# Kernel optimization log

Hardware: AMD Instinct MI355X
Metric: run time of the kernel (lower is better)

## Reference

```python
import jax, jax.numpy as jnp
import numpy as np

E = 16           # num_experts
K = 2            # top-k
NOISE_STD = 1.0 / E
TAU = 1.0
EPS = 1e-8


def setup_inputs() -> dict:
    key = jax.random.key(0)
    k1, k2, k3, k4 = jax.random.split(key, 4)
    B, C, H, W = 128, 512, 32, 32
    x = jax.random.normal(k1, (B, C, H, W), dtype=jnp.float32)
    # nn.Linear(dim, num_experts, bias=False): weight [E, C]
    W_gate = jax.random.normal(k2, (E, C), dtype=jnp.float32) * (1.0 / np.sqrt(C))
    comp = jax.random.uniform(k3, (E,), dtype=jnp.float32, minval=0.5, maxval=1.5)
    complexity = comp / comp.max()  # complexity_scale == 'max'
    noise = jax.random.normal(k4, (B, E), dtype=jnp.float32) * NOISE_STD
    return {"x": x, "W_gate": W_gate, "complexity": complexity, "noise": noise}


def _std_unbiased(a):
    # torch .std() uses ddof=1
    return jnp.std(a, ddof=1)


def _norm_cdf(z):
    return 0.5 * (1.0 + jax.lax.erf(z / np.sqrt(2.0).astype(np.float32)))


def reference(x, W_gate, complexity, noise):
    B = x.shape[0]
    # gate: AdaptiveAvgPool2d(1) -> [B,C] -> Linear -> [B,E]
    pooled = x.mean(axis=(2, 3))                     # [B, C]
    logits = pooled @ W_gate.T                       # [B, E]

    # importance loss (training path)
    importance = jax.nn.softmax(logits, axis=-1).sum(axis=0) * (complexity * TAU)  # [E]
    loss_imp = (_std_unbiased(importance) / (importance.mean() + EPS)) ** 2

    noisy_logits = logits + noise                    # [B, E]
    gating_scores = jax.nn.softmax(noisy_logits, axis=-1)
    top_k_values, top_k_indices = jax.lax.top_k(gating_scores, K)   # [B, K]

    # load loss: prob each expert's noisy logit beats the k-th noisy logit
    _, noisy_idx = jax.lax.top_k(noisy_logits, K)
    thr = jnp.take_along_axis(noisy_logits, noisy_idx[:, K - 1:K], axis=-1)  # [B,1]
    noise_required = (thr - logits) / NOISE_STD      # [B, E]
    p = 1.0 - _norm_cdf(noise_required)
    p_mean = p.mean(axis=0)                          # [E]
    loss_load = (_std_unbiased(p_mean) / (p_mean.mean() + EPS)) ** 2

    aux_loss = 0.5 * loss_imp + 0.5 * loss_load

    # scatter top-k values back into dense [B, E] gates
    rows = jnp.arange(B)[:, None]
    gates = jnp.zeros_like(logits).at[rows, top_k_indices].set(top_k_values)
    return gates, top_k_indices, top_k_values, aux_loss
```

## Files before the change

### kernel.cpp

```cpp
#include <hip/hip_runtime.h>
#include <math.h>

#define BB 128
#define CC 512
#define HW 1024
#define EE 16
#define KK 2
#define INV_NOISE_STD 16.0f
#define EPSV 1e-8f

typedef float vf4 __attribute__((ext_vector_type(4)));

__device__ __forceinline__ float wave_sum(float v) {
    #pragma unroll
    for (int off = 32; off > 0; off >>= 1) v += __shfl_down(v, off, 64);
    return v;
}

__global__ void __launch_bounds__(256) pool_kernel(const float* __restrict__ x,
                                                   float* __restrict__ pooled) {
    int wave = (blockIdx.x * 256 + threadIdx.x) >> 6;
    int lane = threadIdx.x & 63;
    const vf4* p = (const vf4*)(x + (size_t)wave * HW);
    float s = 0.0f;
    #pragma unroll
    for (int j = 0; j < 4; ++j) {
        vf4 v = __builtin_nontemporal_load(&p[lane + 64 * j]);
        s += (v.x + v.y) + (v.z + v.w);
    }
    s = wave_sum(s);
    if (lane == 0) pooled[wave] = s * (1.0f / 1024.0f);
}

__global__ void __launch_bounds__(256) logits_kernel(const float* __restrict__ pooled,
                                                     const float* __restrict__ Wg,
                                                     float* __restrict__ logits) {
    __shared__ float prow[CC];
    int b = blockIdx.x;
    for (int c = threadIdx.x; c < CC; c += 256) prow[c] = pooled[b * CC + c];
    __syncthreads();
    int t = threadIdx.x;
    int e = t >> 4;
    int g = t & 15;
    float s = 0.0f;
    for (int c = g; c < CC; c += 16) s += prow[c] * Wg[e * CC + c];
    #pragma unroll
    for (int off = 8; off > 0; off >>= 1) s += __shfl_down(s, off, 16);
    if (g == 0) logits[b * EE + e] = s;
}

__global__ void __launch_bounds__(128) stats_kernel(const float* __restrict__ logits,
                                                    const float* __restrict__ complexity,
                                                    const float* __restrict__ noise,
                                                    float* __restrict__ out) {
    __shared__ float imp[EE];
    __shared__ float psum[EE];
    int t = threadIdx.x;
    int lane = t & 63;
    if (t < EE) { imp[t] = 0.0f; psum[t] = 0.0f; }
    __syncthreads();

    int b = t;
    float lg[EE], nlg[EE];
    #pragma unroll
    for (int e = 0; e < EE; ++e) lg[e] = logits[b * EE + e];
    #pragma unroll
    for (int e = 0; e < EE; ++e) nlg[e] = lg[e] + noise[b * EE + e];

    float mx = lg[0];
    #pragma unroll
    for (int e = 1; e < EE; ++e) mx = fmaxf(mx, lg[e]);
    float sm[EE]; float se = 0.0f;
    #pragma unroll
    for (int e = 0; e < EE; ++e) { sm[e] = expf(lg[e] - mx); se += sm[e]; }
    float inv_se = 1.0f / se;
    #pragma unroll
    for (int e = 0; e < EE; ++e) {
        float ws = wave_sum(sm[e] * inv_se);
        if (lane == 0) atomicAdd(&imp[e], ws);
    }

    float mxn = nlg[0];
    #pragma unroll
    for (int e = 1; e < EE; ++e) mxn = fmaxf(mxn, nlg[e]);
    float gsc[EE]; float sen = 0.0f;
    #pragma unroll
    for (int e = 0; e < EE; ++e) { gsc[e] = expf(nlg[e] - mxn); sen += gsc[e]; }
    float inv_sen = 1.0f / sen;
    #pragma unroll
    for (int e = 0; e < EE; ++e) gsc[e] *= inv_sen;

    int i1 = 0;
    #pragma unroll
    for (int e = 1; e < EE; ++e) if (nlg[e] > nlg[i1]) i1 = e;
    int i2 = (i1 == 0) ? 1 : 0;
    #pragma unroll
    for (int e = 0; e < EE; ++e) if (e != i1 && e != i2 && nlg[e] > nlg[i2]) i2 = e;
    float thr = nlg[i2];
    float v1 = gsc[i1], v2 = gsc[i2];

    #pragma unroll
    for (int e = 0; e < EE; ++e) {
        float z = (thr - lg[e]) * INV_NOISE_STD;
        float p = 0.5f * erfcf(z * 0.70710678118654752f);
        float ws = wave_sum(p);
        if (lane == 0) atomicAdd(&psum[e], ws);
    }

    #pragma unroll
    for (int e = 0; e < EE; ++e)
        out[b * EE + e] = (e == i1) ? v1 : ((e == i2) ? v2 : 0.0f);
    out[BB * EE + b * KK + 0] = (float)i1;
    out[BB * EE + b * KK + 1] = (float)i2;
    out[BB * EE + BB * KK + b * KK + 0] = v1;
    out[BB * EE + BB * KK + b * KK + 1] = v2;

    __syncthreads();
    if (t == 0) {
        float im[EE]; float mean1 = 0.0f;
        #pragma unroll
        for (int e = 0; e < EE; ++e) { im[e] = imp[e] * complexity[e]; mean1 += im[e]; }
        mean1 *= (1.0f / EE);
        float var1 = 0.0f;
        #pragma unroll
        for (int e = 0; e < EE; ++e) { float d = im[e] - mean1; var1 += d * d; }
        var1 *= (1.0f / (EE - 1));
        float li = var1 / ((mean1 + EPSV) * (mean1 + EPSV));

        float pm[EE]; float mean2 = 0.0f;
        #pragma unroll
        for (int e = 0; e < EE; ++e) { pm[e] = psum[e] * (1.0f / BB); mean2 += pm[e]; }
        mean2 *= (1.0f / EE);
        float var2 = 0.0f;
        #pragma unroll
        for (int e = 0; e < EE; ++e) { float d = pm[e] - mean2; var2 += d * d; }
        var2 *= (1.0f / (EE - 1));
        float ll = var2 / ((mean2 + EPSV) * (mean2 + EPSV));

        out[BB * EE + 2 * BB * KK] = 0.5f * li + 0.5f * ll;
    }
}

extern "C" void kernel_launch(void* const* d_in, const int* in_sizes, int n_in,
                              void* d_out, int out_size, void* d_ws, size_t ws_size,
                              hipStream_t stream) {
    const float* x     = (const float*)d_in[0];
    const float* Wg    = (const float*)d_in[1];
    const float* comp  = (const float*)d_in[2];
    const float* noise = (const float*)d_in[3];
    float* out = (float*)d_out;

    float* pooled = (float*)d_ws;
    float* logits = pooled + BB * CC;

    pool_kernel<<<(BB * CC) / 4, 256, 0, stream>>>(x, pooled);
    logits_kernel<<<BB, 256, 0, stream>>>(pooled, Wg, logits);
    stats_kernel<<<1, 128, 0, stream>>>(logits, comp, noise, out);
}
```

Measured before the change: 356.4 us.

## Fuse logits GEMV and stats into a single one-block kernel

Merges the logits kernel and the stats kernel into one 1024-thread single-block kernel. It loops over the batch in groups of 4 rows, keeps the logits in shared memory and then runs the softmax, top-k and loss stats. This removes one kernel launch and the global round-trip of the logits. In exchange the 128-block GEMV now runs serially in one block over 32 iterations with barriers, so that phase gets longer. The total is dominated by the 256MB pooling pass.

```diff
diff --git a/kernel.cpp b/kernel.cpp
--- a/kernel.cpp
+++ b/kernel.cpp
@@ -32,108 +32,112 @@
     if (lane == 0) pooled[wave] = s * (1.0f / 1024.0f);
 }
 
-__global__ void __launch_bounds__(256) logits_kernel(const float* __restrict__ pooled,
+__global__ void __launch_bounds__(1024) fused_kernel(const float* __restrict__ pooled,
                                                      const float* __restrict__ Wg,
-                                                     float* __restrict__ logits) {
-    __shared__ float prow[CC];
-    int b = blockIdx.x;
-    for (int c = threadIdx.x; c < CC; c += 256) prow[c] = pooled[b * CC + c];
-    __syncthreads();
-    int t = threadIdx.x;
-    int e = t >> 4;
-    int g = t & 15;
-    float s = 0.0f;
-    for (int c = g; c < CC; c += 16) s += prow[c] * Wg[e * CC + c];
-    #pragma unroll
-    for (int off = 8; off > 0; off >>= 1) s += __shfl_down(s, off, 16);
-    if (g == 0) logits[b * EE + e] = s;
-}
-
-__global__ void __launch_bounds__(128) stats_kernel(const float* __restrict__ logits,
-                                                    const float* __restrict__ complexity,
-                                                    const float* __restrict__ noise,
-                                                    float* __restrict__ out) {
+                                                     const float* __restrict__ complexity,
+                                                     const float* __restrict__ noise,
+                                                     float* __restrict__ out) {
+    __shared__ float lsm[BB * EE];
+    __shared__ float prow[4 * CC];
     __shared__ float imp[EE];
     __shared__ float psum[EE];
     int t = threadIdx.x;
-    int lane = t & 63;
+
     if (t < EE) { imp[t] = 0.0f; psum[t] = 0.0f; }
-    __syncthreads();
 
-    int b = t;
-    float lg[EE], nlg[EE];
-    #pragma unroll
-    for (int e = 0; e < EE; ++e) lg[e] = logits[b * EE + e];
-    #pragma unroll
-    for (int e = 0; e < EE; ++e) nlg[e] = lg[e] + noise[b * EE + e];
-
-    float mx = lg[0];
-    #pragma unroll
-    for (int e = 1; e < EE; ++e) mx = fmaxf(mx, lg[e]);
-    float sm[EE]; float se = 0.0f;
-    #pragma unroll
-    for (int e = 0; e < EE; ++e) { sm[e] = expf(lg[e] - mx); se += sm[e]; }
-    float inv_se = 1.0f / se;
-    #pragma unroll
-    for (int e = 0; e < EE; ++e) {
-        float ws = wave_sum(sm[e] * inv_se);
-        if (lane == 0) atomicAdd(&imp[e], ws);
+    int sub = t >> 8;
+    int tt  = t & 255;
+    int e   = tt >> 4;
+    int g   = tt & 15;
+    for (int b0 = 0; b0 < BB; b0 += 4) {
+        for (int c = t; c < 4 * CC; c += 1024)
+            prow[c] = pooled[(size_t)b0 * CC + c];
+        __syncthreads();
+        float s = 0.0f;
+        for (int c = g; c < CC; c += 16) s += prow[sub * CC + c] * Wg[e * CC + c];
+        #pragma unroll
+        for (int off = 8; off > 0; off >>= 1) s += __shfl_down(s, off, 16);
+        if (g == 0) lsm[(b0 + sub) * EE + e] = s;
+        __syncthreads();
     }
 
-    float mxn = nlg[0];
-    #pragma unroll
-    for (int e = 1; e < EE; ++e) mxn = fmaxf(mxn, nlg[e]);
-    float gsc[EE]; float sen = 0.0f;
-    #pragma unroll
-    for (int e = 0; e < EE; ++e) { gsc[e] = expf(nlg[e] - mxn); sen += gsc[e]; }
-    float inv_sen = 1.0f / sen;
-    #pragma unroll
-    for (int e = 0; e < EE; ++e) gsc[e] *= inv_sen;
+    if (t < BB) {
+        int b = t;
+        int lane = t & 63;
+        float lg[EE], nlg[EE];
+        #pragma unroll
+        for (int e2 = 0; e2 < EE; ++e2) lg[e2] = lsm[b * EE + e2];
+        #pragma unroll
+        for (int e2 = 0; e2 < EE; ++e2) nlg[e2] = lg[e2] + noise[b * EE + e2];
 
-    int i1 = 0;
-    #pragma unroll
-    for (int e = 1; e < EE; ++e) if (nlg[e] > nlg[i1]) i1 = e;
-    int i2 = (i1 == 0) ? 1 : 0;
-    #pragma unroll
-    for (int e = 0; e < EE; ++e) if (e != i1 && e != i2 && nlg[e] > nlg[i2]) i2 = e;
-    float thr = nlg[i2];
-    float v1 = gsc[i1], v2 = gsc[i2];
+        float mx = lg[0];
+        #pragma unroll
+        for (int e2 = 1; e2 < EE; ++e2) mx = fmaxf(mx, lg[e2]);
+        float sm[EE]; float se = 0.0f;
+        #pragma unroll
+        for (int e2 = 0; e2 < EE; ++e2) { sm[e2] = expf(lg[e2] - mx); se += sm[e2]; }
+        float inv_se = 1.0f / se;
+        #pragma unroll
+        for (int e2 = 0; e2 < EE; ++e2) {
+            float ws = wave_sum(sm[e2] * inv_se);
+            if (lane == 0) atomicAdd(&imp[e2], ws);
+        }
 
-    #pragma unroll
-    for (int e = 0; e < EE; ++e) {
-        float z = (thr - lg[e]) * INV_NOISE_STD;
-        float p = 0.5f * erfcf(z * 0.70710678118654752f);
-        float ws = wave_sum(p);
-        if (lane == 0) atomicAdd(&psum[e], ws);
+        float mxn = nlg[0];
+        #pragma unroll
+        for (int e2 = 1; e2 < EE; ++e2) mxn = fmaxf(mxn, nlg[e2]);
+        float gsc[EE]; float sen = 0.0f;
+        #pragma unroll
+        for (int e2 = 0; e2 < EE; ++e2) { gsc[e2] = expf(nlg[e2] - mxn); sen += gsc[e2]; }
+        float inv_sen = 1.0f / sen;
+        #pragma unroll
+        for (int e2 = 0; e2 < EE; ++e2) gsc[e2] *= inv_sen;
+
+        int i1 = 0;
+        #pragma unroll
+        for (int e2 = 1; e2 < EE; ++e2) if (nlg[e2] > nlg[i1]) i1 = e2;
+        int i2 = (i1 == 0) ? 1 : 0;
+        #pragma unroll
+        for (int e2 = 0; e2 < EE; ++e2) if (e2 != i1 && e2 != i2 && nlg[e2] > nlg[i2]) i2 = e2;
+        float thr = nlg[i2];
+        float v1 = gsc[i1], v2 = gsc[i2];
+
+        #pragma unroll
+        for (int e2 = 0; e2 < EE; ++e2) {
+            float z = (thr - lg[e2]) * INV_NOISE_STD;
+            float p = 0.5f * erfcf(z * 0.70710678118654752f);
+            float ws = wave_sum(p);
+            if (lane == 0) atomicAdd(&psum[e2], ws);
+        }
+
+        #pragma unroll
+        for (int e2 = 0; e2 < EE; ++e2)
+            out[b * EE + e2] = (e2 == i1) ? v1 : ((e2 == i2) ? v2 : 0.0f);
+        out[BB * EE + b * KK + 0] = (float)i1;
+        out[BB * EE + b * KK + 1] = (float)i2;
+        out[BB * EE + BB * KK + b * KK + 0] = v1;
+        out[BB * EE + BB * KK + b * KK + 1] = v2;
     }
-
-    #pragma unroll
-    for (int e = 0; e < EE; ++e)
-        out[b * EE + e] = (e == i1) ? v1 : ((e == i2) ? v2 : 0.0f);
-    out[BB * EE + b * KK + 0] = (float)i1;
-    out[BB * EE + b * KK + 1] = (float)i2;
-    out[BB * EE + BB * KK + b * KK + 0] = v1;
-    out[BB * EE + BB * KK + b * KK + 1] = v2;
 
     __syncthreads();
     if (t == 0) {
         float im[EE]; float mean1 = 0.0f;
         #pragma unroll
-        for (int e = 0; e < EE; ++e) { im[e] = imp[e] * complexity[e]; mean1 += im[e]; }
+        for (int e2 = 0; e2 < EE; ++e2) { im[e2] = imp[e2] * complexity[e2]; mean1 += im[e2]; }
         mean1 *= (1.0f / EE);
         float var1 = 0.0f;
         #pragma unroll
-        for (int e = 0; e < EE; ++e) { float d = im[e] - mean1; var1 += d * d; }
+        for (int e2 = 0; e2 < EE; ++e2) { float d = im[e2] - mean1; var1 += d * d; }
         var1 *= (1.0f / (EE - 1));
         float li = var1 / ((mean1 + EPSV) * (mean1 + EPSV));
 
         float pm[EE]; float mean2 = 0.0f;
         #pragma unroll
-        for (int e = 0; e < EE; ++e) { pm[e] = psum[e] * (1.0f / BB); mean2 += pm[e]; }
+        for (int e2 = 0; e2 < EE; ++e2) { pm[e2] = psum[e2] * (1.0f / BB); mean2 += pm[e2]; }
         mean2 *= (1.0f / EE);
         float var2 = 0.0f;
         #pragma unroll
-        for (int e = 0; e < EE; ++e) { float d = pm[e] - mean2; var2 += d * d; }
+        for (int e2 = 0; e2 < EE; ++e2) { float d = pm[e2] - mean2; var2 += d * d; }
         var2 *= (1.0f / (EE - 1));
         float ll = var2 / ((mean2 + EPSV) * (mean2 + EPSV));
 
@@ -151,9 +155,7 @@
     float* out = (float*)d_out;
 
     float* pooled = (float*)d_ws;
-    float* logits = pooled + BB * CC;
 
     pool_kernel<<<(BB * CC) / 4, 256, 0, stream>>>(x, pooled);
-    logits_kernel<<<BB, 256, 0, stream>>>(pooled, Wg, logits);
-    stats_kernel<<<1, 128, 0, stream>>>(logits, comp, noise, out);
+    fused_kernel<<<1, 1024, 0, stream>>>(pooled, Wg, comp, noise, out);
 }
```

New measurement: 465.1 us. 1.3x slower.
